# Performance work log

Hardware: AMD Instinct MI355X
Metric: run time of the kernel (lower is better)

The kernel has to match this reference:

```python
import jax, jax.numpy as jnp
import numpy as np

B, S, D = 4, 2048, 1024
H = 16
HD = D // H  # 64

def setup_inputs() -> dict:
    key = jax.random.key(0)
    ks = jax.random.split(key, 4)
    scale = 0.02
    return {
        "hidden_states": jax.random.normal(ks[0], (B, S, D), dtype=jnp.float32),
        "attention_mask": jnp.zeros((B, 1, 1, S), dtype=jnp.float32),
        "Wq": jax.random.normal(ks[1], (D, D), dtype=jnp.float32) * scale,
        "bq": jnp.zeros((D,), dtype=jnp.float32),
        "Wk": jax.random.normal(ks[2], (D, D), dtype=jnp.float32) * scale,
        "bk": jnp.zeros((D,), dtype=jnp.float32),
        "Wv": jax.random.normal(ks[3], (D, D), dtype=jnp.float32) * scale,
        "bv": jnp.zeros((D,), dtype=jnp.float32),
    }

def reference(hidden_states, attention_mask, Wq, bq, Wk, bk, Wv, bv):
    b, s, d = hidden_states.shape
    def proj(W, bias):
        # Linear then split heads: [b, s, d] -> [b, H, s, HD]
        y = hidden_states @ W.T + bias
        return y.reshape(b, s, H, HD).transpose(0, 2, 1, 3)
    Q = proj(Wq, bq)
    K = proj(Wk, bk)
    V = proj(Wv, bv)
    scores = jnp.einsum('bhqd,bhkd->bhqk', Q, K) / jnp.sqrt(jnp.float32(HD))
    scores = scores + attention_mask  # additive mask, broadcast [b,1,1,s]
    probs = jax.nn.softmax(scores, axis=-1)
    # dropout prob = 0.0 (eval-mode): identity
    context = jnp.einsum('bhqk,bhkd->bhqd', probs, V)
    return context.transpose(0, 2, 1, 3).reshape(b, s, d)
```

## Files before the change

kernel.cpp:

```cpp
#include <hip/hip_runtime.h>


typedef short bf16x4 __attribute__((ext_vector_type(4)));
typedef short bf16x8 __attribute__((ext_vector_type(8)));
typedef float f32x4 __attribute__((ext_vector_type(4)));

#define SEQ 2048
#define DIM 1024
#define NH 16
#define HDIM 64
#define QKV_ELEMS ((size_t)64 * SEQ * HDIM)

#define WS_FLAG  50331648ull
#define WS_XBF   50331904ull
#define WS_WBF   67109120ull
#define WS_BF32  73400576ull
#define WS_NEED  73412868ull

#define LOG2E 1.4426950408889634f
#define QSCALE (0.125f * LOG2E)

static __device__ __forceinline__ unsigned short f2bf(float f) {
  union { float f; unsigned u; } x; x.f = f;
  unsigned r = x.u + 0x7fffu + ((x.u >> 16) & 1u);
  return (unsigned short)(r >> 16);
}
static __device__ __forceinline__ float bf2f(unsigned short h) {
  union { unsigned u; float f; } x; x.u = ((unsigned)h) << 16;
  return x.f;
}
static __device__ __forceinline__ unsigned cvtpk(float a, float b) {
  unsigned r;
  asm("v_cvt_pk_bf16_f32 %0, %1, %2" : "=v"(r) : "v"(a), "v"(b));
  return r;
}
static __device__ __forceinline__ int vswz(int s) {
  return (s & ~31) | (((s >> 2) & 3) << 3) | (((s >> 4) & 1) << 2);
}

template <bool FP32>
static __device__ __forceinline__ float load1(const void* p, size_t i) {
  if (FP32) return ((const float*)p)[i];
  else      return bf2f(((const unsigned short*)p)[i]);
}
template <bool FP32>
static __device__ __forceinline__ bf16x8 load8bf(const void* p, size_t i) {
  if (FP32) {
    f32x4 a = *(const f32x4*)((const float*)p + i);
    f32x4 b = *(const f32x4*)((const float*)p + i + 4);
    union { bf16x8 v; unsigned short u[8]; } r;
#pragma unroll
    for (int j = 0; j < 4; ++j) { r.u[j] = f2bf(a[j]); r.u[4 + j] = f2bf(b[j]); }
    return r.v;
  } else {
    return *(const bf16x8*)((const unsigned short*)p + i);
  }
}

static __device__ __forceinline__ void glds16(const unsigned short* g, unsigned short* l) {
  __builtin_amdgcn_global_load_lds(
      (const __attribute__((address_space(1))) unsigned int*)(unsigned long long)(const void*)g,
      (__attribute__((address_space(3))) unsigned int*)(unsigned int)(unsigned long long)(void*)l,
      16, 0, 0);
}

__global__ void detect_dtype(const unsigned short* __restrict__ X, int* __restrict__ flag) {
  __shared__ int zc[256], bc[256];
  int z = 0, b = 0;
  for (int i = threadIdx.x; i < 16384; i += 256) {
    unsigned short u = X[2 * i];
    if (u == 0) z++;
    int e = (u >> 7) & 0xff;
    if (e >= 134) b++;
  }
  zc[threadIdx.x] = z; bc[threadIdx.x] = b;
  __syncthreads();
  for (int s = 128; s > 0; s >>= 1) {
    if (threadIdx.x < s) { zc[threadIdx.x] += zc[threadIdx.x + s]; bc[threadIdx.x] += bc[threadIdx.x + s]; }
    __syncthreads();
  }
  if (threadIdx.x == 0)
    *flag = (zc[0] > 8192 || bc[0] > 64) ? 1 : 0;
}

template <bool FP32>
__global__ void convert_all(const void* __restrict__ X,
                            const void* __restrict__ Wq, const void* __restrict__ Wk,
                            const void* __restrict__ Wv,
                            const void* __restrict__ bq, const void* __restrict__ bk,
                            const void* __restrict__ bv,
                            unsigned char* __restrict__ ws, const int* __restrict__ flag) {
  if (*flag != (FP32 ? 1 : 0)) return;
  unsigned short* Xb = (unsigned short*)(ws + WS_XBF);
  unsigned short* Wb = (unsigned short*)(ws + WS_WBF);
  float* Bb = (float*)(ws + WS_BF32);
  int blk = blockIdx.x;
  if (blk < 4096) {
    size_t base = ((size_t)blk * 256 + threadIdx.x) * 8;
    *(bf16x8*)(Xb + base) = load8bf<FP32>(X, base);
  } else if (blk < 5632) {
    int w = (blk - 4096) >> 9;
    int r = (blk - 4096) & 511;
    const void* W = (w == 0) ? Wq : (w == 1) ? Wk : Wv;
    size_t base = ((size_t)r * 256 + threadIdx.x) * 8;
    *(bf16x8*)(Wb + (size_t)w * 1048576 + base) = load8bf<FP32>(W, base);
  } else {
    int w = blk - 5632;
    const void* Bsrc = (w == 0) ? bq : (w == 1) ? bk : bv;
    for (int i = threadIdx.x; i < 1024; i += 256)
      Bb[w * 1024 + i] = load1<FP32>(Bsrc, i);
  }
}

__global__ __launch_bounds__(256) void qkv_bf(
    const unsigned short* __restrict__ Xb, const unsigned short* __restrict__ Wb,
    const float* __restrict__ Bb,
    unsigned short* __restrict__ Qo, unsigned short* __restrict__ Ko,
    unsigned short* __restrict__ Vo)
{
  const int z = blockIdx.z;
  const unsigned short* W = Wb + (size_t)z * 1048576;

  __shared__ __align__(16) unsigned short Xs[128 * 64];
  __shared__ __align__(16) unsigned short Ws[128 * 64];

  const int tid  = threadIdx.x;
  const int wave = tid >> 6;
  const int lane = tid & 63;
  const int col  = lane & 15;
  const int quad = lane >> 4;
  const int wr = wave & 1;
  const int wc = wave >> 1;
  const int m0 = blockIdx.x * 128;
  const int n0 = blockIdx.y * 128;

  f32x4 zero4 = {0.f, 0.f, 0.f, 0.f};
  f32x4 acc[4][4];
#pragma unroll
  for (int i = 0; i < 4; ++i)
#pragma unroll
    for (int j = 0; j < 4; ++j) acc[i][j] = zero4;

  const int srow8 = lane >> 3;
  const int sseg  = lane & 7;

  for (int k0 = 0; k0 < DIM; k0 += 64) {
    __syncthreads();
#pragma unroll
    for (int a = 0; a < 4; ++a) {
      int rowbase = wave * 32 + a * 8;
      int row = rowbase + srow8;
      int lseg = sseg ^ (row & 7);
      glds16(Xb + (size_t)(m0 + row) * DIM + k0 + lseg * 8, Xs + rowbase * 64);
      glds16(W  + (size_t)(n0 + row) * DIM + k0 + lseg * 8, Ws + rowbase * 64);
    }
    __syncthreads();

#pragma unroll
    for (int kk = 0; kk < 2; ++kk) {
      bf16x8 Af[4], Bf[4];
#pragma unroll
      for (int i = 0; i < 4; ++i) {
        int ra = wr * 64 + i * 16 + col;
        Af[i] = *(const bf16x8*)(Xs + ra * 64 + ((kk * 4 + quad) ^ (ra & 7)) * 8);
        int rb = wc * 64 + i * 16 + col;
        Bf[i] = *(const bf16x8*)(Ws + rb * 64 + ((kk * 4 + quad) ^ (rb & 7)) * 8);
      }
#pragma unroll
      for (int i = 0; i < 4; ++i)
#pragma unroll
        for (int j = 0; j < 4; ++j)
          acc[i][j] = __builtin_amdgcn_mfma_f32_16x16x32_bf16(Af[i], Bf[j], acc[i][j], 0, 0, 0);
    }
  }

  const float oscale = (z == 0) ? QSCALE : 1.0f;
  if (z < 2) {
    unsigned short* Yo = (z == 0) ? Qo : Ko;
#pragma unroll
    for (int i = 0; i < 4; ++i) {
#pragma unroll
      for (int j = 0; j < 4; ++j) {
        int n = n0 + wc * 64 + j * 16 + col;
        float bvf = Bb[z * 1024 + n];
        int h = n >> 6, hd = n & 63;
#pragma unroll
        for (int r = 0; r < 4; ++r) {
          int m = m0 + wr * 64 + i * 16 + quad * 4 + r;
          int b = m >> 11, s = m & 2047;
          Yo[((size_t)(b * NH + h) * SEQ + s) * HDIM + hd] = f2bf((acc[i][j][r] + bvf) * oscale);
        }
      }
    }
  } else {
#pragma unroll
    for (int i = 0; i < 4; ++i) {
#pragma unroll
      for (int j = 0; j < 4; ++j) {
        int n = n0 + wc * 64 + j * 16 + col;
        float bvf = Bb[2 * 1024 + n];
        int h = n >> 6, hd = n & 63;
        int mbase = m0 + wr * 64 + i * 16 + quad * 4;
        int b = mbase >> 11, s = mbase & 2047;
        unsigned long long pk = 0;
#pragma unroll
        for (int r = 0; r < 4; ++r)
          pk |= (unsigned long long)f2bf(acc[i][j][r] + bvf) << (16 * r);
        *(unsigned long long*)(Vo + ((size_t)(b * NH + h) * HDIM + hd) * SEQ + vswz(s)) = pk;
      }
    }
  }
}

#define XS_STRIDE 40
template <bool FP32>
__global__ __launch_bounds__(256) void qkv_any(
    const void* __restrict__ X,
    const void* __restrict__ Wq, const void* __restrict__ bq,
    const void* __restrict__ Wk, const void* __restrict__ bk,
    const void* __restrict__ Wv, const void* __restrict__ bv,
    unsigned short* __restrict__ Qo, unsigned short* __restrict__ Ko,
    unsigned short* __restrict__ Vo, const int* __restrict__ flag)
{
  if (*flag != (FP32 ? 1 : 0)) return;
  const int z = blockIdx.z;
  const void* W    = (z == 0) ? Wq : (z == 1) ? Wk : Wv;
  const void* bias = (z == 0) ? bq : (z == 1) ? bk : bv;

  __shared__ __align__(16) unsigned short Xs[128 * XS_STRIDE];
  __shared__ __align__(16) unsigned short Ws[128 * XS_STRIDE];

  const int tid  = threadIdx.x;
  const int wave = tid >> 6;
  const int lane = tid & 63;
  const int col  = lane & 15;
  const int quad = lane >> 4;
  const int wr = wave & 1;
  const int wc = wave >> 1;
  const int m0 = blockIdx.x * 128;
  const int n0 = blockIdx.y * 128;

  f32x4 zero4 = {0.f, 0.f, 0.f, 0.f};
  f32x4 acc[4][4];
#pragma unroll
  for (int i = 0; i < 4; ++i)
#pragma unroll
    for (int j = 0; j < 4; ++j) acc[i][j] = zero4;

  const int srow = tid >> 2;
  const int sseg = (tid & 3) << 3;

  for (int k0 = 0; k0 < DIM; k0 += 32) {
    __syncthreads();
#pragma unroll
    for (int a = 0; a < 2; ++a) {
      int r = a * 64 + srow;
      *(bf16x8*)(Xs + r * XS_STRIDE + sseg) = load8bf<FP32>(X, (size_t)(m0 + r) * DIM + k0 + sseg);
      *(bf16x8*)(Ws + r * XS_STRIDE + sseg) = load8bf<FP32>(W, (size_t)(n0 + r) * DIM + k0 + sseg);
    }
    __syncthreads();

    bf16x8 Af[4], Bf[4];
#pragma unroll
    for (int i = 0; i < 4; ++i)
      Af[i] = *(const bf16x8*)(Xs + (wr * 64 + i * 16 + col) * XS_STRIDE + quad * 8);
#pragma unroll
    for (int j = 0; j < 4; ++j)
      Bf[j] = *(const bf16x8*)(Ws + (wc * 64 + j * 16 + col) * XS_STRIDE + quad * 8);
#pragma unroll
    for (int i = 0; i < 4; ++i)
#pragma unroll
      for (int j = 0; j < 4; ++j)
        acc[i][j] = __builtin_amdgcn_mfma_f32_16x16x32_bf16(Af[i], Bf[j], acc[i][j], 0, 0, 0);
  }

  const float oscale = (z == 0) ? QSCALE : 1.0f;
  if (z < 2) {
    unsigned short* Yo = (z == 0) ? Qo : Ko;
#pragma unroll
    for (int i = 0; i < 4; ++i) {
#pragma unroll
      for (int j = 0; j < 4; ++j) {
        int n = n0 + wc * 64 + j * 16 + col;
        float bvf = load1<FP32>(bias, n);
        int h = n >> 6, hd = n & 63;
#pragma unroll
        for (int r = 0; r < 4; ++r) {
          int m = m0 + wr * 64 + i * 16 + quad * 4 + r;
          int b = m >> 11, s = m & 2047;
          Yo[((size_t)(b * NH + h) * SEQ + s) * HDIM + hd] = f2bf((acc[i][j][r] + bvf) * oscale);
        }
      }
    }
  } else {
#pragma unroll
    for (int i = 0; i < 4; ++i) {
#pragma unroll
      for (int j = 0; j < 4; ++j) {
        int n = n0 + wc * 64 + j * 16 + col;
        float bvf = load1<FP32>(bias, n);
        int h = n >> 6, hd = n & 63;
        int mbase = m0 + wr * 64 + i * 16 + quad * 4;
        int b = mbase >> 11, s = mbase & 2047;
        unsigned long long pk = 0;
#pragma unroll
        for (int r = 0; r < 4; ++r)
          pk |= (unsigned long long)f2bf(acc[i][j][r] + bvf) << (16 * r);
        *(unsigned long long*)(Vo + ((size_t)(b * NH + h) * HDIM + hd) * SEQ + vswz(s)) = pk;
      }
    }
  }
}

template <bool FP32>
__global__ __launch_bounds__(512, 2) void attn_kernel(
    const unsigned short* __restrict__ Q,
    const unsigned short* __restrict__ K,
    const unsigned short* __restrict__ Vt,
    const void* __restrict__ mask,
    void* __restrict__ OutV, const int* __restrict__ flag)
{
  if (*flag != (FP32 ? 1 : 0)) return;

  __shared__ __align__(16) unsigned short Ks[2 * 128 * 64];
  __shared__ __align__(16) unsigned short Vs[2 * 64 * 128];
  __shared__ __align__(16) float Msall[SEQ];

  const int tid  = threadIdx.x;
  const int wave = tid >> 6;
  const int lane = tid & 63;
  const int col  = lane & 15;
  const int quad = lane >> 4;
  const int qt = blockIdx.x;
  const int bh = blockIdx.y;
  const int b  = bh >> 4;
  const int h  = bh & 15;

  const unsigned short* Qb = Q  + (size_t)bh * SEQ * HDIM;
  const unsigned short* Kb = K  + (size_t)bh * SEQ * HDIM;
  const unsigned short* Vb = Vt + (size_t)bh * HDIM * SEQ;

  {
    if (FP32) {
      f32x4 a = *(const f32x4*)((const float*)mask + (size_t)b * SEQ + tid * 4);
#pragma unroll
      for (int j = 0; j < 4; ++j) a[j] *= LOG2E;
      *(f32x4*)(Msall + tid * 4) = a;
    } else {
      bf16x4 v = *(const bf16x4*)((const unsigned short*)mask + (size_t)b * SEQ + tid * 4);
      f32x4 a;
#pragma unroll
      for (int j = 0; j < 4; ++j) a[j] = bf2f((unsigned short)v[j]) * LOG2E;
      *(f32x4*)(Msall + tid * 4) = a;
    }
  }

  const int qrow0 = qt * 256 + wave * 32 + col;
  const int qrow1 = qrow0 + 16;
  const bf16x8 Qf00 = *(const bf16x8*)(Qb + (size_t)qrow0 * HDIM + quad * 8);
  const bf16x8 Qf01 = *(const bf16x8*)(Qb + (size_t)qrow0 * HDIM + 32 + quad * 8);
  const bf16x8 Qf10 = *(const bf16x8*)(Qb + (size_t)qrow1 * HDIM + quad * 8);
  const bf16x8 Qf11 = *(const bf16x8*)(Qb + (size_t)qrow1 * HDIM + 32 + quad * 8);

  const f32x4 z4 = {0.f, 0.f, 0.f, 0.f};
  f32x4 Oacc0[4], Oacc1[4];
  f32x4 Osum0 = z4, Osum1 = z4;
#pragma unroll
  for (int t = 0; t < 4; ++t) { Oacc0[t] = z4; Oacc1[t] = z4; }
  float mrun0 = -1e30f, mrun1 = -1e30f;

  union { bf16x8 v; unsigned u[4]; } ones;
#pragma unroll
  for (int i = 0; i < 4; ++i) ones.u[i] = 0x3F803F80u;

  const int krow_in = lane >> 3;
  const int kphys   = lane & 7;
  const int klseg   = kphys ^ krow_in;
  const unsigned short* kSrc0 = Kb + (size_t)(wave * 16 + 0 + krow_in) * HDIM + klseg * 8;
  const unsigned short* kSrc1 = Kb + (size_t)(wave * 16 + 8 + krow_in) * HDIM + klseg * 8;
  const int vrow_in = lane >> 4;
  const int vphys   = lane & 15;
  const int vrowA0  = wave * 8 + 0 + vrow_in;
  const int vrowA1  = wave * 8 + 4 + vrow_in;
  const unsigned short* vSrc0 = Vb + (size_t)vrowA0 * SEQ + (vphys ^ (vrowA0 & 15)) * 8;
  const unsigned short* vSrc1 = Vb + (size_t)vrowA1 * SEQ + (vphys ^ (vrowA1 & 15)) * 8;

  auto stage = [&](int ktn, int bufn) {
    unsigned short* Kdst = Ks + bufn * (128 * 64) + (wave * 16) * 64;
    unsigned short* Vdst = Vs + bufn * (64 * 128) + (wave * 8) * 128;
    const size_t ko = (size_t)ktn * 128 * HDIM;
    const size_t vo = (size_t)ktn * 128;
    glds16(kSrc0 + ko, Kdst);
    glds16(kSrc1 + ko, Kdst + 8 * 64);
    glds16(vSrc0 + vo, Vdst);
    glds16(vSrc1 + vo, Vdst + 4 * 128);
  };

  stage(0, 0);

  for (int kt = 0; kt < 16; ++kt) {
    __syncthreads();
    if (kt < 15) stage(kt + 1, (kt + 1) & 1);

    const unsigned short* Kcur = Ks + (kt & 1) * (128 * 64);
    const unsigned short* Vcur = Vs + (kt & 1) * (64 * 128);
    const float* Mc = Msall + kt * 128;

    f32x4 st0[8], st1[8];
    __builtin_amdgcn_s_setprio(1);
#pragma unroll
    for (int t = 0; t < 8; ++t) {
      const unsigned short* kr = Kcur + (t * 16 + col) * 64;
      bf16x8 Ka = *(const bf16x8*)(kr + (quad ^ (col & 7)) * 8);
      bf16x8 Kc = *(const bf16x8*)(kr + ((4 + quad) ^ (col & 7)) * 8);
      f32x4 c = *(const f32x4*)(Mc + t * 16 + quad * 4);
      f32x4 d0 = c, d1 = c;
      d0 = __builtin_amdgcn_mfma_f32_16x16x32_bf16(Ka, Qf00, d0, 0, 0, 0);
      d0 = __builtin_amdgcn_mfma_f32_16x16x32_bf16(Kc, Qf01, d0, 0, 0, 0);
      d1 = __builtin_amdgcn_mfma_f32_16x16x32_bf16(Ka, Qf10, d1, 0, 0, 0);
      d1 = __builtin_amdgcn_mfma_f32_16x16x32_bf16(Kc, Qf11, d1, 0, 0, 0);
      st0[t] = d0; st1[t] = d1;
    }
    __builtin_amdgcn_s_setprio(0);

    float pm0, pm1;
    {
      f32x4 m40, m41;
#pragma unroll
      for (int r = 0; r < 4; ++r) {
        float a0 = fmaxf(fmaxf(st0[0][r], st0[1][r]), st0[2][r]);
        a0 = fmaxf(fmaxf(a0, st0[3][r]), st0[4][r]);
        a0 = fmaxf(fmaxf(a0, st0[5][r]), st0[6][r]);
        m40[r] = fmaxf(a0, st0[7][r]);
        float a1 = fmaxf(fmaxf(st1[0][r], st1[1][r]), st1[2][r]);
        a1 = fmaxf(fmaxf(a1, st1[3][r]), st1[4][r]);
        a1 = fmaxf(fmaxf(a1, st1[5][r]), st1[6][r]);
        m41[r] = fmaxf(a1, st1[7][r]);
      }
      pm0 = fmaxf(fmaxf(fmaxf(m40[0], m40[1]), m40[2]), m40[3]);
      pm1 = fmaxf(fmaxf(fmaxf(m41[0], m41[1]), m41[2]), m41[3]);
    }
    pm0 = fmaxf(pm0, __shfl_xor(pm0, 16, 64));
    pm0 = fmaxf(pm0, __shfl_xor(pm0, 32, 64));
    pm1 = fmaxf(pm1, __shfl_xor(pm1, 16, 64));
    pm1 = fmaxf(pm1, __shfl_xor(pm1, 32, 64));

    if (!__all((pm0 - mrun0 <= 8.0f) && (pm1 - mrun1 <= 8.0f))) {
      float mn0 = fmaxf(mrun0, pm0), mn1 = fmaxf(mrun1, pm1);
      float a0 = __builtin_amdgcn_exp2f(mrun0 - mn0);
      float a1 = __builtin_amdgcn_exp2f(mrun1 - mn1);
      mrun0 = mn0; mrun1 = mn1;
      float av0[4], av1[4];
#pragma unroll
      for (int r = 0; r < 4; ++r) {
        av0[r] = __shfl(a0, quad * 4 + r, 64);
        av1[r] = __shfl(a1, quad * 4 + r, 64);
      }
#pragma unroll
      for (int t = 0; t < 4; ++t)
#pragma unroll
        for (int r = 0; r < 4; ++r) {
          Oacc0[t][r] *= av0[r];
          Oacc1[t][r] *= av1[r];
        }
#pragma unroll
      for (int r = 0; r < 4; ++r) { Osum0[r] *= av0[r]; Osum1[r] *= av1[r]; }
    }

#pragma unroll
    for (int t = 0; t < 8; ++t)
#pragma unroll
      for (int r = 0; r < 4; ++r) {
        st0[t][r] = __builtin_amdgcn_exp2f(st0[t][r] - mrun0);
        st1[t][r] = __builtin_amdgcn_exp2f(st1[t][r] - mrun1);
      }

    __builtin_amdgcn_s_setprio(1);
#pragma unroll
    for (int tp = 0; tp < 4; ++tp) {
      union { bf16x8 v; unsigned u[4]; } A0, A1;
      A0.u[0] = cvtpk(st0[2 * tp][0],     st0[2 * tp][1]);
      A0.u[1] = cvtpk(st0[2 * tp][2],     st0[2 * tp][3]);
      A0.u[2] = cvtpk(st0[2 * tp + 1][0], st0[2 * tp + 1][1]);
      A0.u[3] = cvtpk(st0[2 * tp + 1][2], st0[2 * tp + 1][3]);
      A1.u[0] = cvtpk(st1[2 * tp][0],     st1[2 * tp][1]);
      A1.u[1] = cvtpk(st1[2 * tp][2],     st1[2 * tp][3]);
      A1.u[2] = cvtpk(st1[2 * tp + 1][0], st1[2 * tp + 1][1]);
      A1.u[3] = cvtpk(st1[2 * tp + 1][2], st1[2 * tp + 1][3]);
      Osum0 = __builtin_amdgcn_mfma_f32_16x16x32_bf16(A0.v, ones.v, Osum0, 0, 0, 0);
      Osum1 = __builtin_amdgcn_mfma_f32_16x16x32_bf16(A1.v, ones.v, Osum1, 0, 0, 0);
#pragma unroll
      for (int t2 = 0; t2 < 4; ++t2) {
        bf16x8 Bv = *(const bf16x8*)(Vcur + (t2 * 16 + col) * 128 + ((tp * 4 + quad) ^ col) * 8);
        Oacc0[t2] = __builtin_amdgcn_mfma_f32_16x16x32_bf16(A0.v, Bv, Oacc0[t2], 0, 0, 0);
        Oacc1[t2] = __builtin_amdgcn_mfma_f32_16x16x32_bf16(A1.v, Bv, Oacc1[t2], 0, 0, 0);
      }
    }
    __builtin_amdgcn_s_setprio(0);
  }

  float liv0[4], liv1[4];
#pragma unroll
  for (int r = 0; r < 4; ++r) { liv0[r] = 1.0f / Osum0[r]; liv1[r] = 1.0f / Osum1[r]; }
#pragma unroll
  for (int t2 = 0; t2 < 4; ++t2) {
#pragma unroll
    for (int r = 0; r < 4; ++r) {
      int q0 = qt * 256 + wave * 32 + quad * 4 + r;
      int q1 = q0 + 16;
      float v0 = Oacc0[t2][r] * liv0[r];
      float v1 = Oacc1[t2][r] * liv1[r];
      v0 = (v0 == v0) ? v0 : 0.0f;
      v1 = (v1 == v1) ? v1 : 0.0f;
      size_t o0 = ((size_t)b * SEQ + q0) * DIM + h * HDIM + t2 * 16 + col;
      size_t o1 = ((size_t)b * SEQ + q1) * DIM + h * HDIM + t2 * 16 + col;
      if (FP32) {
        ((float*)OutV)[o0] = v0;
        ((float*)OutV)[o1] = v1;
      } else {
        ((unsigned short*)OutV)[o0] = f2bf(v0);
        ((unsigned short*)OutV)[o1] = f2bf(v1);
      }
    }
  }
}

extern "C" void kernel_launch(void* const* d_in, const int* in_sizes, int n_in,
                              void* d_out, int out_size, void* d_ws, size_t ws_size,
                              hipStream_t stream) {
  const void* X    = d_in[0];
  const void* mask = d_in[1];
  const void* Wq   = d_in[2];
  const void* bq   = d_in[3];
  const void* Wk   = d_in[4];
  const void* bk   = d_in[5];
  const void* Wv   = d_in[6];
  const void* bv   = d_in[7];

  unsigned char* ws = (unsigned char*)d_ws;
  unsigned short* Qw = (unsigned short*)ws;
  unsigned short* Kw = Qw + QKV_ELEMS;
  unsigned short* Vw = Kw + QKV_ELEMS;
  int* flag = (int*)(ws + WS_FLAG);

  detect_dtype<<<1, 256, 0, stream>>>((const unsigned short*)X, flag);

  if (ws_size >= WS_NEED) {
    convert_all<false><<<5635, 256, 0, stream>>>(X, Wq, Wk, Wv, bq, bk, bv, ws, flag);
    convert_all<true ><<<5635, 256, 0, stream>>>(X, Wq, Wk, Wv, bq, bk, bv, ws, flag);
    qkv_bf<<<dim3(64, 8, 3), 256, 0, stream>>>(
        (const unsigned short*)(ws + WS_XBF), (const unsigned short*)(ws + WS_WBF),
        (const float*)(ws + WS_BF32), Qw, Kw, Vw);
  } else {
    qkv_any<false><<<dim3(64, 8, 3), 256, 0, stream>>>(X, Wq, bq, Wk, bk, Wv, bv, Qw, Kw, Vw, flag);
    qkv_any<true ><<<dim3(64, 8, 3), 256, 0, stream>>>(X, Wq, bq, Wk, bk, Wv, bv, Qw, Kw, Vw, flag);
  }

  attn_kernel<false><<<dim3(8, 64), 512, 0, stream>>>(Qw, Kw, Vw, mask, d_out, flag);
  attn_kernel<true ><<<dim3(8, 64), 512, 0, stream>>>(Qw, Kw, Vw, mask, d_out, flag);
}
```

Baseline: 278.3 us.

## Merge dtype-templated launches into runtime-flag kernels and remap QKV GEMM blocks

Replaces the paired FP32/bf16 templated launches of convert and attention kernels with single kernels that branch on the runtime dtype flag, removing two redundant early-exit launches. The dtype detection kernel samples fewer elements with more threads and scaled thresholds. The QKV GEMM grid is flattened to 1D with a block index remap that interleaves blocks across XCDs for better L2 locality. Runtime branching may add some register pressure or code in the attention kernel, and the sparser dtype sampling may be less robust.

```diff
diff --git a/kernel.cpp b/kernel.cpp
--- a/kernel.cpp
+++ b/kernel.cpp
@@ -56,6 +56,9 @@
     return *(const bf16x8*)((const unsigned short*)p + i);
   }
 }
+static __device__ __forceinline__ bf16x8 load8bf_rt(const void* p, size_t i, bool fp32) {
+  return fp32 ? load8bf<true>(p, i) : load8bf<false>(p, i);
+}
 
 static __device__ __forceinline__ void glds16(const unsigned short* g, unsigned short* l) {
   __builtin_amdgcn_global_load_lds(
@@ -65,50 +68,49 @@
 }
 
 __global__ void detect_dtype(const unsigned short* __restrict__ X, int* __restrict__ flag) {
-  __shared__ int zc[256], bc[256];
+  __shared__ int zc[1024], bc[1024];
   int z = 0, b = 0;
-  for (int i = threadIdx.x; i < 16384; i += 256) {
-    unsigned short u = X[2 * i];
+  for (int i = threadIdx.x; i < 4096; i += 1024) {
+    unsigned short u = X[8 * i];
     if (u == 0) z++;
     int e = (u >> 7) & 0xff;
     if (e >= 134) b++;
   }
   zc[threadIdx.x] = z; bc[threadIdx.x] = b;
   __syncthreads();
-  for (int s = 128; s > 0; s >>= 1) {
+  for (int s = 512; s > 0; s >>= 1) {
     if (threadIdx.x < s) { zc[threadIdx.x] += zc[threadIdx.x + s]; bc[threadIdx.x] += bc[threadIdx.x + s]; }
     __syncthreads();
   }
   if (threadIdx.x == 0)
-    *flag = (zc[0] > 8192 || bc[0] > 64) ? 1 : 0;
-}
-
-template <bool FP32>
-__global__ void convert_all(const void* __restrict__ X,
-                            const void* __restrict__ Wq, const void* __restrict__ Wk,
-                            const void* __restrict__ Wv,
-                            const void* __restrict__ bq, const void* __restrict__ bk,
-                            const void* __restrict__ bv,
-                            unsigned char* __restrict__ ws, const int* __restrict__ flag) {
-  if (*flag != (FP32 ? 1 : 0)) return;
+    *flag = (zc[0] > 2048 || bc[0] > 16) ? 1 : 0;
+}
+
+__global__ void convert_all_u(const void* __restrict__ X,
+                              const void* __restrict__ Wq, const void* __restrict__ Wk,
+                              const void* __restrict__ Wv,
+                              const void* __restrict__ bq, const void* __restrict__ bk,
+                              const void* __restrict__ bv,
+                              unsigned char* __restrict__ ws, const int* __restrict__ flag) {
+  const bool fp32 = (*flag != 0);
   unsigned short* Xb = (unsigned short*)(ws + WS_XBF);
   unsigned short* Wb = (unsigned short*)(ws + WS_WBF);
   float* Bb = (float*)(ws + WS_BF32);
   int blk = blockIdx.x;
   if (blk < 4096) {
     size_t base = ((size_t)blk * 256 + threadIdx.x) * 8;
-    *(bf16x8*)(Xb + base) = load8bf<FP32>(X, base);
+    *(bf16x8*)(Xb + base) = load8bf_rt(X, base, fp32);
   } else if (blk < 5632) {
     int w = (blk - 4096) >> 9;
     int r = (blk - 4096) & 511;
     const void* W = (w == 0) ? Wq : (w == 1) ? Wk : Wv;
     size_t base = ((size_t)r * 256 + threadIdx.x) * 8;
-    *(bf16x8*)(Wb + (size_t)w * 1048576 + base) = load8bf<FP32>(W, base);
+    *(bf16x8*)(Wb + (size_t)w * 1048576 + base) = load8bf_rt(W, base, fp32);
   } else {
     int w = blk - 5632;
     const void* Bsrc = (w == 0) ? bq : (w == 1) ? bk : bv;
     for (int i = threadIdx.x; i < 1024; i += 256)
-      Bb[w * 1024 + i] = load1<FP32>(Bsrc, i);
+      Bb[w * 1024 + i] = fp32 ? load1<true>(Bsrc, i) : load1<false>(Bsrc, i);
   }
 }
 
@@ -118,7 +120,12 @@
     unsigned short* __restrict__ Qo, unsigned short* __restrict__ Ko,
     unsigned short* __restrict__ Vo)
 {
-  const int z = blockIdx.z;
+  const int bid = blockIdx.x;
+  const int wg  = (bid & 7) * 192 + (bid >> 3);
+  const int z   = wg / 512;
+  const int rem = wg - z * 512;
+  const int nb  = rem >> 6;
+  const int mb  = rem & 63;
   const unsigned short* W = Wb + (size_t)z * 1048576;
 
   __shared__ __align__(16) unsigned short Xs[128 * 64];
@@ -131,8 +138,8 @@
   const int quad = lane >> 4;
   const int wr = wave & 1;
   const int wc = wave >> 1;
-  const int m0 = blockIdx.x * 128;
-  const int n0 = blockIdx.y * 128;
+  const int m0 = mb * 128;
+  const int n0 = nb * 128;
 
   f32x4 zero4 = {0.f, 0.f, 0.f, 0.f};
   f32x4 acc[4][4];
@@ -312,7 +319,6 @@
   }
 }
 
-template <bool FP32>
 __global__ __launch_bounds__(512, 2) void attn_kernel(
     const unsigned short* __restrict__ Q,
     const unsigned short* __restrict__ K,
@@ -320,7 +326,7 @@
     const void* __restrict__ mask,
     void* __restrict__ OutV, const int* __restrict__ flag)
 {
-  if (*flag != (FP32 ? 1 : 0)) return;
+  const bool fp32 = (*flag != 0);
 
   __shared__ __align__(16) unsigned short Ks[2 * 128 * 64];
   __shared__ __align__(16) unsigned short Vs[2 * 64 * 128];
@@ -341,7 +347,7 @@
   const unsigned short* Vb = Vt + (size_t)bh * HDIM * SEQ;
 
   {
-    if (FP32) {
+    if (fp32) {
       f32x4 a = *(const f32x4*)((const float*)mask + (size_t)b * SEQ + tid * 4);
 #pragma unroll
       for (int j = 0; j < 4; ++j) a[j] *= LOG2E;
@@ -514,7 +520,7 @@
       v1 = (v1 == v1) ? v1 : 0.0f;
       size_t o0 = ((size_t)b * SEQ + q0) * DIM + h * HDIM + t2 * 16 + col;
       size_t o1 = ((size_t)b * SEQ + q1) * DIM + h * HDIM + t2 * 16 + col;
-      if (FP32) {
+      if (fp32) {
         ((float*)OutV)[o0] = v0;
         ((float*)OutV)[o1] = v1;
       } else {
@@ -543,12 +549,11 @@
   unsigned short* Vw = Kw + QKV_ELEMS;
   int* flag = (int*)(ws + WS_FLAG);
 
-  detect_dtype<<<1, 256, 0, stream>>>((const unsigned short*)X, flag);
+  detect_dtype<<<1, 1024, 0, stream>>>((const unsigned short*)X, flag);
 
   if (ws_size >= WS_NEED) {
-    convert_all<false><<<5635, 256, 0, stream>>>(X, Wq, Wk, Wv, bq, bk, bv, ws, flag);
-    convert_all<true ><<<5635, 256, 0, stream>>>(X, Wq, Wk, Wv, bq, bk, bv, ws, flag);
-    qkv_bf<<<dim3(64, 8, 3), 256, 0, stream>>>(
+    convert_all_u<<<5635, 256, 0, stream>>>(X, Wq, Wk, Wv, bq, bk, bv, ws, flag);
+    qkv_bf<<<1536, 256, 0, stream>>>(
         (const unsigned short*)(ws + WS_XBF), (const unsigned short*)(ws + WS_WBF),
         (const float*)(ws + WS_BF32), Qw, Kw, Vw);
   } else {
@@ -556,6 +561,5 @@
     qkv_any<true ><<<dim3(64, 8, 3), 256, 0, stream>>>(X, Wq, bq, Wk, bk, Wv, bv, Qw, Kw, Vw, flag);
   }
 
-  attn_kernel<false><<<dim3(8, 64), 512, 0, stream>>>(Qw, Kw, Vw, mask, d_out, flag);
-  attn_kernel<true ><<<dim3(8, 64), 512, 0, stream>>>(Qw, Kw, Vw, mask, d_out, flag);
-}
+  attn_kernel<<<dim3(8, 64), 512, 0, stream>>>(Qw, Kw, Vw, mask, d_out, flag);
+}
```

Measured after the change: 262.9 us. 1.06x faster.
